# Kernel tuning notes

Hardware: AMD Instinct MI355X
Metric: run time of the kernel (lower is better)

Reference implementation:

```python
import jax, jax.numpy as jnp
import numpy as np

LEAK = 0.2
EPS = 1e-8


def _mod_conv(x, style, weight):
    # x: [B,C,H,W], style: [B,C], weight: [O,C,k,k]
    b, c, h, w = x.shape
    o, _, k, _ = weight.shape
    # per-sample modulation + demodulation (StyleGAN2 style)
    wmod = weight[None] * (style[:, None, :, None, None] + 1.0)  # [B,O,C,k,k]
    d = jax.lax.rsqrt(jnp.sum(wmod * wmod, axis=(2, 3, 4), keepdims=True) + EPS)
    wmod = wmod * d
    pad = (k - 1) // 2  # same padding for stride=1, dilation=1
    xg = x.reshape(1, b * c, h, w)
    wg = wmod.reshape(b * o, c, k, k)
    y = jax.lax.conv_general_dilated(
        xg, wg, window_strides=(1, 1), padding=[(pad, pad), (pad, pad)],
        dimension_numbers=('NCHW', 'OIHW', 'NCHW'), feature_group_count=b)
    return y.reshape(b, o, h, w)


def setup_inputs() -> dict:
    key = jax.random.key(0)
    ks = jax.random.split(key, 8)
    B, LAT, CIN, F, H, W = 8, 512, 256, 256, 64, 64
    K = 3
    kaiming = lambda k, shape, fan_in: jax.random.normal(k, shape, jnp.float32) * np.sqrt(2.0 / fan_in)
    return {
        'x': jax.random.normal(ks[0], (B, CIN, H, W), jnp.float32),
        'istyle': jax.random.normal(ks[1], (B, LAT), jnp.float32),
        'ws1': jax.random.normal(ks[2], (CIN, LAT), jnp.float32) * (1.0 / np.sqrt(LAT)),
        'bs1': jnp.zeros((CIN,), jnp.float32),
        'conv1_w': kaiming(ks[3], (F, CIN, K, K), CIN * K * K),
        'ws2': jax.random.normal(ks[4], (F, LAT), jnp.float32) * (1.0 / np.sqrt(LAT)),
        'bs2': jnp.zeros((F,), jnp.float32),
        'conv2_w': kaiming(ks[5], (F, F, K, K), F * K * K),
    }


def reference(x, istyle, ws1, bs1, conv1_w, ws2, bs2, conv2_w):
    b, c, h, w = x.shape
    # bilinear upsample x2, align_corners=False (half-pixel centers)
    x = jax.image.resize(x, (b, c, 2 * h, 2 * w), method='bilinear')
    s1 = istyle @ ws1.T + bs1
    x = _mod_conv(x, s1, conv1_w)
    x = jax.nn.leaky_relu(x, LEAK)
    s2 = istyle @ ws2.T + bs2
    x = _mod_conv(x, s2, conv2_w)
    return jax.nn.leaky_relu(x, LEAK)
```

## Files before the change

### kernel.cpp

```cpp
#include <hip/hip_runtime.h>

typedef __bf16 bf16x8 __attribute__((ext_vector_type(8)));
typedef float f32x4 __attribute__((ext_vector_type(4)));


#define GLDS(gsrc, ldst) __builtin_amdgcn_global_load_lds( \
    (const __attribute__((address_space(1))) unsigned int*)(gsrc), \
    (__attribute__((address_space(3))) unsigned int*)(ldst), 16, 0, 0)

#define MFMA(a, b, c) __builtin_amdgcn_mfma_f32_16x16x32_bf16((a), (b), (c), 0, 0, 0)

__global__ void style_kernel(const float* __restrict__ istyle,
                             const float* __restrict__ ws1, const float* __restrict__ bs1,
                             const float* __restrict__ ws2, const float* __restrict__ bs2,
                             float* __restrict__ sbuf) {
    int b = blockIdx.x;
    int which = blockIdx.y;
    int c = threadIdx.x;
    const float* ws = which ? ws2 : ws1;
    const float* bs = which ? bs2 : bs1;
    __shared__ float st[512];
    for (int i = threadIdx.x; i < 512; i += 256) st[i] = istyle[b * 512 + i];
    __syncthreads();
    float acc = bs[c];
    const float* wr = ws + (size_t)c * 512;
    for (int l = 0; l < 512; ++l) acc += st[l] * wr[l];
    sbuf[((size_t)which * 8 + b) * 256 + c] = acc;
}

__global__ void modw_kernel(const float* __restrict__ w, const float* __restrict__ s,
                            __bf16* __restrict__ wm) {
    int wv = threadIdx.x >> 6, lane = threadIdx.x & 63;
    int idx = blockIdx.x * 4 + wv;
    int b = idx >> 8, o = idx & 255;
    int c0 = lane * 4;
    const float* wr = w + ((size_t)o * 256 + c0) * 9;
    const float* sb = s + (size_t)b * 256 + c0;
    float v[36];
    float ss = 0.f;
#pragma unroll
    for (int cc = 0; cc < 4; ++cc) {
        float sm = sb[cc] + 1.0f;
#pragma unroll
        for (int t = 0; t < 9; ++t) {
            float x = wr[cc * 9 + t] * sm;
            v[cc * 9 + t] = x;
            ss += x * x;
        }
    }
#pragma unroll
    for (int off = 32; off > 0; off >>= 1) ss += __shfl_xor(ss, off);
    float d = rsqrtf(ss + 1e-8f);
    __bf16* wp = wm + ((size_t)(b * 256 + o) * 9) * 256 + c0;
#pragma unroll
    for (int t = 0; t < 9; ++t) {
        union { __bf16 h[4]; uint2 u; } pk;
#pragma unroll
        for (int cc = 0; cc < 4; ++cc) pk.h[cc] = (__bf16)(v[cc * 9 + t] * d);
        *(uint2*)(wp + (size_t)t * 256) = pk.u;
    }
}

__global__ void zeropad_kernel(__bf16* __restrict__ xu, __bf16* __restrict__ y1) {
    int p0 = blockIdx.x * 8;
    int b  = blockIdx.y;
    __bf16* buf = blockIdx.z ? y1 : xu;
    int p = p0 + (threadIdx.x >> 5);
    if (p >= 516) return;
    int chunk = threadIdx.x & 31;
    int y, x;
    if (p < 130)      { y = 0;           x = p; }
    else if (p < 260) { y = 129;         x = p - 130; }
    else if (p < 388) { y = p - 260 + 1; x = 0; }
    else              { y = p - 388 + 1; x = 129; }
    uint4 z = make_uint4(0, 0, 0, 0);
    *(uint4*)(buf + (((size_t)b * 130 + y) * 130 + x) * 256 + chunk * 8) = z;
}

__global__ __launch_bounds__(256) void upsample_kernel(const float* __restrict__ x,
                                                       __bf16* __restrict__ xu) {
    int y = blockIdx.x;
    int b = blockIdx.y;
    __shared__ __bf16 orow[128 * 256];
    int tid = threadIdx.x;

    int j = y >> 1;
    int y0, y1; float wy0, wy1;
    if (y & 1) { y0 = j; y1 = (j + 1 < 64) ? j + 1 : 63; wy0 = 0.75f; wy1 = 0.25f; }
    else       { y0 = (j - 1 >= 0) ? j - 1 : 0; y1 = j; wy0 = 0.25f; wy1 = 0.75f; }

    int c  = tid >> 3;
    int xs = (tid & 7) * 16;
    for (int ct = 0; ct < 8; ++ct) {
        int cc = ct * 32 + c;
        const float* row0 = x + ((size_t)(b * 256 + cc) * 64 + y0) * 64;
        const float* row1 = x + ((size_t)(b * 256 + cc) * 64 + y1) * 64;
#pragma unroll
        for (int k = 0; k < 16; ++k) {
            int xo = xs + k;
            int i = xo >> 1;
            int x0, x1; float wx0, wx1;
            if (xo & 1) { x0 = i; x1 = (i + 1 < 64) ? i + 1 : 63; wx0 = 0.75f; wx1 = 0.25f; }
            else        { x0 = (i - 1 >= 0) ? i - 1 : 0; x1 = i; wx0 = 0.25f; wx1 = 0.75f; }
            float v0 = wx0 * row0[x0] + wx1 * row0[x1];
            float v1 = wx0 * row1[x0] + wx1 * row1[x1];
            orow[xo * 256 + cc] = (__bf16)(wy0 * v0 + wy1 * v1);
        }
    }
    __syncthreads();
    uint4* dst = (uint4*)(xu + (((size_t)(b * 130) + y + 1) * 130 + 1) * 256);
    const uint4* src = (const uint4*)orow;
#pragma unroll
    for (int it = 0; it < 16; ++it)
        dst[it * 256 + tid] = src[it * 256 + tid];
}

template <int PHASE>
__global__ __launch_bounds__(256, 2) void conv_kernel(
    const __bf16* __restrict__ in,
    const __bf16* __restrict__ wmall,
    float* __restrict__ outf,
    __bf16* __restrict__ outb) {
    __shared__ __attribute__((aligned(128))) char smem[65536];
    const int tid  = threadIdx.x;
    const int bid  = blockIdx.x;
    const int swz  = (bid & 7) * 128 + (bid >> 3);
    const int b    = swz >> 7;
    const int yrow = swz & 127;
    const int lane = tid & 63;
    const int wv   = tid >> 6;
    const int wo   = (wv >> 1) * 128;
    const int wn   = (wv & 1) * 64;
    const int arow = lane & 15;
    const int cgb  = lane >> 4;
    const int xsw  = (cgb ^ ((arow >> 1) & 3)) * 16;
    const int srow   = wv * 16 + (lane >> 2);
    const int chunkS = (lane & 3) ^ ((lane >> 3) & 3);
    const __bf16* wm_b = wmall + (size_t)b * 256 * 2304;
    const __bf16* arow_base = wm_b + (size_t)srow * 2304 + chunkS * 8;
    const __bf16* brow_base = in + ((size_t)((b * 130 + yrow) * 130 + srow)) * 256 + chunkS * 8;
    const int ldsA = (wv * 16) * 32;
    const int ldsB = (wv * 16) * 32;

    f32x4 acc[8][4] = {};

#define STAGE(tt, buf)                                                          \
    {   const int tap = (tt) % 9, cb = (tt) / 9;                                \
        const size_t aoff = (size_t)(tap * 256 + cb * 32);                      \
        const size_t boff = (size_t)(((tap / 3) * 130 + (tap % 3)) * 256 + cb * 32); \
        __bf16* Ad = (__bf16*)smem + (buf) * 8192 + ldsA;                       \
        __bf16* Bd = (__bf16*)(smem + 32768) + (buf) * 4096 + ldsB;             \
        _Pragma("unroll")                                                       \
        for (int q = 0; q < 4; ++q)                                             \
            GLDS(arow_base + aoff + (size_t)q * 64 * 2304, Ad + q * 64 * 32);   \
        _Pragma("unroll")                                                       \
        for (int q = 0; q < 2; ++q)                                             \
            GLDS(brow_base + boff + (size_t)q * 64 * 256, Bd + q * 64 * 32);    \
    }

    STAGE(0, 0);
    asm volatile("s_waitcnt vmcnt(0)" ::: "memory");
    __builtin_amdgcn_s_barrier();
    asm volatile("" ::: "memory");

    for (int t = 0; t < 72; ++t) {
        const int cur = t & 1;
        if (t < 71) STAGE(t + 1, cur ^ 1);
        const char* Ab = smem + cur * 16384 + (wo + arow) * 64 + xsw;
        const char* Bb = smem + 32768 + cur * 8192 + (wn + arow) * 64 + xsw;
        bf16x8 af[8], bfr[4];
#pragma unroll
        for (int jj = 0; jj < 4; ++jj) bfr[jj] = *(const bf16x8*)(Bb + jj * 1024);
#pragma unroll
        for (int m = 0; m < 8; ++m) af[m] = *(const bf16x8*)(Ab + m * 1024);
        __builtin_amdgcn_s_setprio(1);
#pragma unroll
        for (int m = 0; m < 8; ++m)
#pragma unroll
            for (int jj = 0; jj < 4; ++jj)
                acc[m][jj] = MFMA(af[m], bfr[jj], acc[m][jj]);
        __builtin_amdgcn_s_setprio(0);
        asm volatile("s_waitcnt vmcnt(0)" ::: "memory");
        __builtin_amdgcn_s_barrier();
        asm volatile("" ::: "memory");
    }
#undef STAGE

    __builtin_amdgcn_sched_barrier(0);
    __syncthreads();

    if (PHASE == 1) {
        __bf16* const ot = (__bf16*)smem;
        const int cg = lane >> 4;
#pragma unroll
        for (int m = 0; m < 8; ++m)
#pragma unroll
            for (int jj = 0; jj < 4; ++jj) {
                int n  = wn + jj * 16 + arow;
                int ob = (wo + m * 16 + cg * 4) * 2;
                union { __bf16 v[4]; uint2 u; } pk;
#pragma unroll
                for (int r = 0; r < 4; ++r) {
                    float v = acc[m][jj][r];
                    pk.v[r] = (__bf16)((v > 0.f) ? v : 0.2f * v);
                }
                *(uint2*)((char*)ot + n * 512 + (ob ^ ((n & 7) << 4))) = pk.u;
            }
        __syncthreads();
        const int half = lane >> 5;
        const int l32  = lane & 31;
#pragma unroll
        for (int it = 0; it < 16; ++it) {
            int n = wv * 32 + it * 2 + half;
            uint4 v = *(const uint4*)((const char*)ot + n * 512 + ((l32 * 16) ^ ((n & 7) << 4)));
            *(uint4*)(outb + (((size_t)(b * 130) + yrow + 1) * 130 + n + 1) * 256 + l32 * 8) = v;
        }
    } else {
#pragma unroll
        for (int m = 0; m < 8; ++m)
#pragma unroll
            for (int jj = 0; jj < 4; ++jj) {
                int o_base = wo + m * 16 + (lane >> 4) * 4;
                int n      = wn + jj * 16 + (lane & 15);
#pragma unroll
                for (int r = 0; r < 4; ++r) {
                    float v = acc[m][jj][r];
                    v = (v > 0.f) ? v : 0.2f * v;
                    outf[((size_t)(b * 256 + o_base + r) * 128 + yrow) * 128 + n] = v;
                }
            }
    }
}

extern "C" void kernel_launch(void* const* d_in, const int* in_sizes, int n_in,
                              void* d_out, int out_size, void* d_ws, size_t ws_size,
                              hipStream_t stream) {
    const float* x      = (const float*)d_in[0];
    const float* istyle = (const float*)d_in[1];
    const float* ws1    = (const float*)d_in[2];
    const float* bs1    = (const float*)d_in[3];
    const float* w1     = (const float*)d_in[4];
    const float* ws2    = (const float*)d_in[5];
    const float* bs2    = (const float*)d_in[6];
    const float* w2     = (const float*)d_in[7];
    float* out = (float*)d_out;

    char* ws = (char*)d_ws;
    __bf16* xu_p = (__bf16*)(ws);
    __bf16* y1_p = (__bf16*)(ws + 69222400);
    __bf16* wm   = (__bf16*)(ws + 138444800);
    float*  sbuf = (float*)(ws + 147881984);

    style_kernel<<<dim3(8, 2), 256, 0, stream>>>(istyle, ws1, bs1, ws2, bs2, sbuf);
    zeropad_kernel<<<dim3(65, 8, 2), 256, 0, stream>>>(xu_p, y1_p);
    upsample_kernel<<<dim3(128, 8), 256, 0, stream>>>(x, xu_p);
    modw_kernel<<<dim3(512), 256, 0, stream>>>(w1, sbuf, wm);
    conv_kernel<1><<<dim3(1024), 256, 0, stream>>>(xu_p, wm, nullptr, y1_p);
    modw_kernel<<<dim3(512), 256, 0, stream>>>(w2, sbuf + 2048, wm);
    conv_kernel<2><<<dim3(1024), 256, 0, stream>>>(y1_p, wm, out, nullptr);
}
```

Measured before the change: 427.5 us.

## Triple-buffer LDS stages so loads run two iterations ahead of MFMA

```diff
diff --git a/kernel.cpp b/kernel.cpp
--- a/kernel.cpp
+++ b/kernel.cpp
@@ -121,7 +121,7 @@
     const __bf16* __restrict__ wmall,
     float* __restrict__ outf,
     __bf16* __restrict__ outb) {
-    __shared__ __attribute__((aligned(128))) char smem[65536];
+    __shared__ __attribute__((aligned(128))) char smem[73728];
     const int tid  = threadIdx.x;
     const int bid  = blockIdx.x;
     const int swz  = (bid & 7) * 128 + (bid >> 3);
@@ -132,47 +132,51 @@
     const int wo   = (wv >> 1) * 128;
     const int wn   = (wv & 1) * 64;
     const int arow = lane & 15;
-    const int cgb  = lane >> 4;
-    const int xsw  = (cgb ^ ((arow >> 1) & 3)) * 16;
-    const int srow   = wv * 16 + (lane >> 2);
+    const int cg   = lane >> 4;
+    const int swR  = (cg ^ ((arow >> 1) & 3)) << 4;
+    const int r16    = lane >> 2;
     const int chunkS = (lane & 3) ^ ((lane >> 3) & 3);
-    const __bf16* wm_b = wmall + (size_t)b * 256 * 2304;
-    const __bf16* arow_base = wm_b + (size_t)srow * 2304 + chunkS * 8;
-    const __bf16* brow_base = in + ((size_t)((b * 130 + yrow) * 130 + srow)) * 256 + chunkS * 8;
-    const int ldsA = (wv * 16) * 32;
-    const int ldsB = (wv * 16) * 32;
+    const __bf16* aSrc = wmall + ((size_t)b * 256 + wv * 64 + r16) * 2304 + chunkS * 8;
+    const __bf16* bSrc = in + ((size_t)((b * 130 + yrow) * 130) + wv * 32 + r16) * 256 + chunkS * 8;
 
     f32x4 acc[8][4] = {};
 
-#define STAGE(tt, buf)                                                          \
-    {   const int tap = (tt) % 9, cb = (tt) / 9;                                \
-        const size_t aoff = (size_t)(tap * 256 + cb * 32);                      \
-        const size_t boff = (size_t)(((tap / 3) * 130 + (tap % 3)) * 256 + cb * 32); \
-        __bf16* Ad = (__bf16*)smem + (buf) * 8192 + ldsA;                       \
-        __bf16* Bd = (__bf16*)(smem + 32768) + (buf) * 4096 + ldsB;             \
+#define STAGE(tt, bsel)                                                         \
+    {   const int tap_ = (tt) % 9, cb_ = (tt) / 9;                              \
+        const size_t ao_ = (size_t)(tap_ * 256 + cb_ * 32);                     \
+        const size_t bo_ = (size_t)(((tap_ / 3) * 130 + (tap_ % 3)) * 256 + cb_ * 32); \
+        __bf16* Ad_ = (__bf16*)(smem + (bsel) * 24576) + (wv * 64) * 32;        \
+        __bf16* Bd_ = (__bf16*)(smem + (bsel) * 24576 + 16384) + (wv * 32) * 32; \
         _Pragma("unroll")                                                       \
         for (int q = 0; q < 4; ++q)                                             \
-            GLDS(arow_base + aoff + (size_t)q * 64 * 2304, Ad + q * 64 * 32);   \
+            GLDS(aSrc + ao_ + (size_t)q * 16 * 2304, Ad_ + q * 16 * 32);        \
         _Pragma("unroll")                                                       \
         for (int q = 0; q < 2; ++q)                                             \
-            GLDS(brow_base + boff + (size_t)q * 64 * 256, Bd + q * 64 * 32);    \
+            GLDS(bSrc + bo_ + (size_t)q * 16 * 256,  Bd_ + q * 16 * 32);        \
     }
 
     STAGE(0, 0);
-    asm volatile("s_waitcnt vmcnt(0)" ::: "memory");
+    STAGE(1, 1);
+    asm volatile("s_waitcnt vmcnt(6)" ::: "memory");
     __builtin_amdgcn_s_barrier();
     asm volatile("" ::: "memory");
 
     for (int t = 0; t < 72; ++t) {
-        const int cur = t & 1;
-        if (t < 71) STAGE(t + 1, cur ^ 1);
-        const char* Ab = smem + cur * 16384 + (wo + arow) * 64 + xsw;
-        const char* Bb = smem + 32768 + cur * 8192 + (wn + arow) * 64 + xsw;
+        const int bsel = t % 3;
+        const char* Ab = smem + bsel * 24576;
+        const char* Bb = Ab + 16384;
         bf16x8 af[8], bfr[4];
 #pragma unroll
-        for (int jj = 0; jj < 4; ++jj) bfr[jj] = *(const bf16x8*)(Bb + jj * 1024);
-#pragma unroll
-        for (int m = 0; m < 8; ++m) af[m] = *(const bf16x8*)(Ab + m * 1024);
+        for (int jj = 0; jj < 4; ++jj)
+            bfr[jj] = *(const bf16x8*)(Bb + (wn + jj * 16 + arow) * 64 + swR);
+#pragma unroll
+        for (int m = 0; m < 8; ++m)
+            af[m] = *(const bf16x8*)(Ab + (wo + m * 16 + arow) * 64 + swR);
+        asm volatile("s_waitcnt lgkmcnt(0)" ::: "memory");
+        __builtin_amdgcn_sched_barrier(0);
+        __builtin_amdgcn_s_barrier();
+        asm volatile("" ::: "memory");
+        if (t < 70) STAGE(t + 2, (t + 2) % 3);
         __builtin_amdgcn_s_setprio(1);
 #pragma unroll
         for (int m = 0; m < 8; ++m)
@@ -180,9 +184,12 @@
             for (int jj = 0; jj < 4; ++jj)
                 acc[m][jj] = MFMA(af[m], bfr[jj], acc[m][jj]);
         __builtin_amdgcn_s_setprio(0);
-        asm volatile("s_waitcnt vmcnt(0)" ::: "memory");
-        __builtin_amdgcn_s_barrier();
-        asm volatile("" ::: "memory");
+        if (t < 70)      { asm volatile("s_waitcnt vmcnt(6)" ::: "memory"); }
+        else if (t == 70){ asm volatile("s_waitcnt vmcnt(0)" ::: "memory"); }
+        if (t < 71) {
+            __builtin_amdgcn_s_barrier();
+            asm volatile("" ::: "memory");
+        }
     }
 #undef STAGE
 
@@ -191,7 +198,6 @@
 
     if (PHASE == 1) {
         __bf16* const ot = (__bf16*)smem;
-        const int cg = lane >> 4;
 #pragma unroll
         for (int m = 0; m < 8; ++m)
 #pragma unroll
@@ -220,8 +226,8 @@
         for (int m = 0; m < 8; ++m)
 #pragma unroll
             for (int jj = 0; jj < 4; ++jj) {
-                int o_base = wo + m * 16 + (lane >> 4) * 4;
-                int n      = wn + jj * 16 + (lane & 15);
+                int o_base = wo + m * 16 + cg * 4;
+                int n      = wn + jj * 16 + arow;
 #pragma unroll
                 for (int r = 0; r < 4; ++r) {
                     float v = acc[m][jj][r];
```

After: 427.6 us. Within noise of the previous version (+0.0%).
